# Kernel tuning notes

Measured on AMD Instinct MI355X. Metric: run time of the kernel, lower is better.

The kernel has to match this reference:

```python
import jax, jax.numpy as jnp
import numpy as np

H = 64  # hidden_layers

def _lstm_cell(x, h, c, Wih, Whh, bih, bhh):
    # PyTorch LSTMCell: gates ordered i, f, g, o
    gates = x @ Wih.T + bih + h @ Whh.T + bhh  # (B, 4H)
    i, f, g, o = jnp.split(gates, 4, axis=-1)
    c_new = jax.nn.sigmoid(f) * c + jax.nn.sigmoid(i) * jnp.tanh(g)
    h_new = jax.nn.sigmoid(o) * jnp.tanh(c_new)
    return h_new, c_new

def setup_inputs() -> dict:
    key = jax.random.key(0)
    ks = jax.random.split(key, 12)
    B, S = 1024, 512
    s1 = 1.0 / np.sqrt(H)
    u = lambda k, shape: jax.random.uniform(k, shape, jnp.float32, -s1, s1)
    return {
        "input_t": jax.random.normal(ks[0], (B, S), jnp.float32),
        "W_ih1": u(ks[1], (4 * H, 1)),
        "W_hh1": u(ks[2], (4 * H, H)),
        "b_ih1": u(ks[3], (4 * H,)),
        "b_hh1": u(ks[4], (4 * H,)),
        "W_ih2": u(ks[5], (4 * H, H)),
        "W_hh2": u(ks[6], (4 * H, H)),
        "b_ih2": u(ks[7], (4 * H,)),
        "b_hh2": u(ks[8], (4 * H,)),
        "W_lin": u(ks[9], (1, H)),
        "b_lin": u(ks[10], (1,)),
        "future_preds": 0,
    }

def reference(input_t, W_ih1, W_hh1, b_ih1, b_hh1, W_ih2, W_hh2, b_ih2, b_hh2,
              W_lin, b_lin, future_preds):
    B = input_t.shape[0]
    z = jnp.zeros((B, H), jnp.float32)

    def step(carry, x_t):
        h1, c1, h2, c2 = carry
        h1, c1 = _lstm_cell(x_t, h1, c1, W_ih1, W_hh1, b_ih1, b_hh1)
        h2, c2 = _lstm_cell(h1, h2, c2, W_ih2, W_hh2, b_ih2, b_hh2)
        out = h2 @ W_lin.T + b_lin  # (B, 1)
        return (h1, c1, h2, c2), out[:, 0]

    xs = input_t.T[:, :, None]  # (S, B, 1)
    carry, outs = jax.lax.scan(step, (z, z, z, z), xs)
    outputs = outs.T  # (B, S)

    if future_preds > 0:  # static Python int
        def step_ar(carry_o, _):
            (h1, c1, h2, c2), out = carry_o
            h1, c1 = _lstm_cell(out, h1, c1, W_ih1, W_hh1, b_ih1, b_hh1)
            h2, c2 = _lstm_cell(h1, h2, c2, W_ih2, W_hh2, b_ih2, b_hh2)
            out = h2 @ W_lin.T + b_lin
            return ((h1, c1, h2, c2), out), out[:, 0]

        last = outs[-1][:, None]  # (B, 1)
        _, outs2 = jax.lax.scan(step_ar, (carry, last), None, length=future_preds)
        outputs = jnp.concatenate([outputs, outs2.T], axis=1)
    return outputs
```

## Files before the change

### kernel.cpp

```cpp
#include <hip/hip_runtime.h>
#include <stdint.h>

#define HD   64
#define SEQ  512
#define BTCH 1024
#define NB   16
#define NBLK (BTCH / NB)
#define HSTR 72
#define XSTR 513

typedef _Float16 f16x8 __attribute__((ext_vector_type(8)));
typedef float    f32x4 __attribute__((ext_vector_type(4)));

union FragU { uint32_t u[4]; uint4 q; f16x8 v; };

static __device__ __forceinline__ float rcpf_(float x) {
#if __has_builtin(__builtin_amdgcn_rcpf)
    return __builtin_amdgcn_rcpf(x);
#else
    return 1.0f / x;
#endif
}
static __device__ __forceinline__ float sigmoidf_(float x) {
    return rcpf_(1.0f + __expf(-x));
}
static __device__ __forceinline__ float tanhf_(float x) {
    float e = __expf(2.0f * x);
    return (e - 1.0f) * rcpf_(e + 1.0f);
}
static __device__ __forceinline__ uint32_t pack2h(float a, float b) {
    _Float16 ha = (_Float16)a, hb = (_Float16)b;
    uint16_t ua = __builtin_bit_cast(uint16_t, ha);
    uint16_t ub = __builtin_bit_cast(uint16_t, hb);
    return (uint32_t)ua | ((uint32_t)ub << 16);
}

static __device__ __forceinline__ f16x8 make_frag(const float* __restrict__ W,
                                                  int row, int kb) {
    const float* p = W + row * HD + kb;
    FragU f;
    f.u[0] = pack2h(p[0], p[1]);
    f.u[1] = pack2h(p[2], p[3]);
    f.u[2] = pack2h(p[4], p[5]);
    f.u[3] = pack2h(p[6], p[7]);
    return f.v;
}

static __device__ __forceinline__ f16x8 read_B(const uint16_t* Hb, int n, int kb) {
    FragU f;
    f.q = *(const uint4*)(Hb + n * HSTR + kb);
    return f.v;
}

__global__ __attribute__((amdgpu_flat_work_group_size(512, 512)))
void lstm_mfma(const float* __restrict__ input,
               const float* __restrict__ Wih1,
               const float* __restrict__ Whh1,
               const float* __restrict__ bih1, const float* __restrict__ bhh1,
               const float* __restrict__ Wih2,
               const float* __restrict__ Whh2,
               const float* __restrict__ bih2, const float* __restrict__ bhh2,
               const float* __restrict__ Wlin,
               const float* __restrict__ blin,
               float* __restrict__ out)
{
    const int tid  = threadIdx.x;
    const int lane = tid & 63;
    const int wv   = tid >> 6;
    const int ub   = wv & 3;
    const int kc   = wv >> 2;
    const int n    = lane & 15;
    const int l4   = lane >> 4;
    const int b0   = blockIdx.x * NB;

    __shared__ float    xbuf[NB * XSTR];
    __shared__ float    obuf[NB * XSTR];
    __shared__ uint16_t H1[NB * HSTR];
    __shared__ uint16_t H2[NB * HSTR];
    __shared__ f32x4    xchg[4][4][64];
    __shared__ float    perW[4][16];

    for (int i = tid; i < NB * SEQ; i += 512) {
        int nn = i >> 9, tt = i & 511;
        xbuf[nn * XSTR + tt] = input[(size_t)(b0 + nn) * SEQ + tt];
    }
    for (int i = tid; i < NB * HSTR; i += 512) { H1[i] = 0; H2[i] = 0; }

    const int kb = kc * 32 + l4 * 8;
    f16x8 A1[4], A2[4], A3[4];
#pragma unroll
    for (int g = 0; g < 4; ++g) {
        int row = (g * 4 + ub) * 16 + n;
        A1[g] = make_frag(Whh1, row, kb);
        A2[g] = make_frag(Wih2, row, kb);
        A3[g] = make_frag(Whh2, row, kb);
    }

    const int u0 = ub * 16 + l4 * 4;
    f32x4 bias1f[4], wih1f[4], bias2f[4];
    if (kc == 1) {
#pragma unroll
        for (int g = 0; g < 4; ++g)
#pragma unroll
            for (int r = 0; r < 4; ++r) {
                int row = g * 64 + u0 + r;
                bias1f[g][r] = bih1[row] + bhh1[row];
                wih1f[g][r]  = Wih1[row];
            }
    } else {
#pragma unroll
        for (int g = 0; g < 4; ++g)
#pragma unroll
            for (int r = 0; r < 4; ++r) {
                int row = g * 64 + u0 + r;
                bias2f[g][r] = bih2[row] + bhh2[row];
            }
    }
    float wl0 = 0.f, wl1 = 0.f, wl2 = 0.f, wl3 = 0.f;
    if (kc == 0) { wl0 = Wlin[u0]; wl1 = Wlin[u0 + 1]; wl2 = Wlin[u0 + 2]; wl3 = Wlin[u0 + 3]; }
    const float bl = blin[0];
    float c1[4] = {0.f, 0.f, 0.f, 0.f};
    float c2[4] = {0.f, 0.f, 0.f, 0.f};
    const f32x4 zero4 = {0.f, 0.f, 0.f, 0.f};

    __syncthreads();

#pragma unroll 1
    for (int t = 0; t < SEQ; ++t) {
        f16x8 B1 = read_B(H1, n, kb);
        f32x4 acc[4];
        if (kc == 1) {
            float x = xbuf[n * XSTR + t];
#pragma unroll
            for (int g = 0; g < 4; ++g) acc[g] = bias1f[g] + x * wih1f[g];
        } else {
#pragma unroll
            for (int g = 0; g < 4; ++g) acc[g] = zero4;
        }
#pragma unroll
        for (int g = 0; g < 4; ++g)
            acc[g] = __builtin_amdgcn_mfma_f32_16x16x32_f16(A1[g], B1, acc[g], 0, 0, 0);

        if (kc == 1) {
#pragma unroll
            for (int g = 0; g < 4; ++g) xchg[ub][g][lane] = acc[g];
        }
        __syncthreads();

        if (kc == 0) {
#pragma unroll
            for (int g = 0; g < 4; ++g) acc[g] += xchg[ub][g][lane];
            float h1v[4];
#pragma unroll
            for (int r = 0; r < 4; ++r) {
                float i_ = sigmoidf_(acc[0][r]);
                float f_ = sigmoidf_(acc[1][r]);
                float g_ = tanhf_(acc[2][r]);
                float o_ = sigmoidf_(acc[3][r]);
                c1[r] = f_ * c1[r] + i_ * g_;
                h1v[r] = o_ * tanhf_(c1[r]);
            }
            uint2 hw; hw.x = pack2h(h1v[0], h1v[1]); hw.y = pack2h(h1v[2], h1v[3]);
            *(uint2*)(&H1[n * HSTR + u0]) = hw;
        }
        __syncthreads();

        f16x8 B2 = read_B(H1, n, kb);
        f16x8 B3 = read_B(H2, n, kb);
        if (kc == 0) {
#pragma unroll
            for (int g = 0; g < 4; ++g) acc[g] = bias2f[g];
        } else {
#pragma unroll
            for (int g = 0; g < 4; ++g) acc[g] = zero4;
        }
#pragma unroll
        for (int g = 0; g < 4; ++g) {
            acc[g] = __builtin_amdgcn_mfma_f32_16x16x32_f16(A2[g], B2, acc[g], 0, 0, 0);
            acc[g] = __builtin_amdgcn_mfma_f32_16x16x32_f16(A3[g], B3, acc[g], 0, 0, 0);
        }
        if (kc == 1) {
#pragma unroll
            for (int g = 0; g < 4; ++g) xchg[ub][g][lane] = acc[g];
        }
        __syncthreads();

        if (kc == 0) {
#pragma unroll
            for (int g = 0; g < 4; ++g) acc[g] += xchg[ub][g][lane];
            float h2v[4];
#pragma unroll
            for (int r = 0; r < 4; ++r) {
                float i_ = sigmoidf_(acc[0][r]);
                float f_ = sigmoidf_(acc[1][r]);
                float g_ = tanhf_(acc[2][r]);
                float o_ = sigmoidf_(acc[3][r]);
                c2[r] = f_ * c2[r] + i_ * g_;
                h2v[r] = o_ * tanhf_(c2[r]);
            }
            uint2 hw; hw.x = pack2h(h2v[0], h2v[1]); hw.y = pack2h(h2v[2], h2v[3]);
            *(uint2*)(&H2[n * HSTR + u0]) = hw;
            float p = h2v[0] * wl0 + h2v[1] * wl1 + h2v[2] * wl2 + h2v[3] * wl3;
            p += __shfl_xor(p, 16, 64);
            p += __shfl_xor(p, 32, 64);
            if (l4 == 0) perW[ub][n] = p;
        }
        __syncthreads();

        if (wv == 0) {
            float s = perW[0][n] + perW[1][n] + perW[2][n] + perW[3][n] + bl;
            if (lane < 16) obuf[n * XSTR + t] = s;
        }
    }

    __syncthreads();
    for (int i = tid; i < NB * SEQ; i += 512) {
        int nn = i >> 9, tt = i & 511;
        out[(size_t)(b0 + nn) * SEQ + tt] = obuf[nn * XSTR + tt];
    }
}

extern "C" void kernel_launch(void* const* d_in, const int* in_sizes, int n_in,
                              void* d_out, int out_size, void* d_ws, size_t ws_size,
                              hipStream_t stream) {
    const float* input = (const float*)d_in[0];
    const float* Wih1  = (const float*)d_in[1];
    const float* Whh1  = (const float*)d_in[2];
    const float* bih1  = (const float*)d_in[3];
    const float* bhh1  = (const float*)d_in[4];
    const float* Wih2  = (const float*)d_in[5];
    const float* Whh2  = (const float*)d_in[6];
    const float* bih2  = (const float*)d_in[7];
    const float* bhh2  = (const float*)d_in[8];
    const float* Wlin  = (const float*)d_in[9];
    const float* blin  = (const float*)d_in[10];

    float* outp = (float*)d_out;

    lstm_mfma<<<dim3(NBLK), dim3(512), 0, stream>>>(
        input, Wih1, Whh1, bih1, bhh1, Wih2, Whh2, bih2, bhh2, Wlin, blin, outp);
}
```

Measured before the change: 834.5 us.

## Replace K-split reduction with redundant full-K MMA per wave pair

Each pair of waves now computes the full 64-wide K reduction on its own, doubling the MFMA work, instead of splitting K across the pair and exchanging partial sums through shared memory. The gate nonlinearity work is split so each wave handles two of the four output rows. This removes the xchg round-trip and one barrier per step, and lets all waves do useful activation work. Input is now read directly from global memory, prefetched one step ahead, and outputs are written straight to global, which drops the large shared staging buffers. The kernel is also pinned to two waves per EU; the costs are twice the register footprint for the A fragments and many small uncoalesced global stores.

```diff
diff --git a/kernel.cpp b/kernel.cpp
--- a/kernel.cpp
+++ b/kernel.cpp
@@ -7,7 +7,6 @@
 #define NB   16
 #define NBLK (BTCH / NB)
 #define HSTR 72
-#define XSTR 513
 
 typedef _Float16 f16x8 __attribute__((ext_vector_type(8)));
 typedef float    f32x4 __attribute__((ext_vector_type(4)));
@@ -52,7 +51,8 @@
     return f.v;
 }
 
-__global__ __attribute__((amdgpu_flat_work_group_size(512, 512)))
+__global__ __attribute__((amdgpu_flat_work_group_size(512, 512),
+                          amdgpu_waves_per_eu(2, 2)))
 void lstm_mfma(const float* __restrict__ input,
                const float* __restrict__ Wih1,
                const float* __restrict__ Whh1,
@@ -68,155 +68,117 @@
     const int lane = tid & 63;
     const int wv   = tid >> 6;
     const int ub   = wv & 3;
-    const int kc   = wv >> 2;
+    const int hf   = wv >> 2;
     const int n    = lane & 15;
     const int l4   = lane >> 4;
     const int b0   = blockIdx.x * NB;
-
-    __shared__ float    xbuf[NB * XSTR];
-    __shared__ float    obuf[NB * XSTR];
+    const int u0   = ub * 16 + l4 * 4;
+
     __shared__ uint16_t H1[NB * HSTR];
     __shared__ uint16_t H2[NB * HSTR];
-    __shared__ f32x4    xchg[4][4][64];
-    __shared__ float    perW[4][16];
-
-    for (int i = tid; i < NB * SEQ; i += 512) {
-        int nn = i >> 9, tt = i & 511;
-        xbuf[nn * XSTR + tt] = input[(size_t)(b0 + nn) * SEQ + tt];
-    }
+    __shared__ float    perW[8][16];
+
     for (int i = tid; i < NB * HSTR; i += 512) { H1[i] = 0; H2[i] = 0; }
 
-    const int kb = kc * 32 + l4 * 8;
-    f16x8 A1[4], A2[4], A3[4];
+    f16x8 A1[4][2], A2[4][2], A3[4][2];
 #pragma unroll
     for (int g = 0; g < 4; ++g) {
         int row = (g * 4 + ub) * 16 + n;
-        A1[g] = make_frag(Whh1, row, kb);
-        A2[g] = make_frag(Wih2, row, kb);
-        A3[g] = make_frag(Whh2, row, kb);
+#pragma unroll
+        for (int h = 0; h < 2; ++h) {
+            int kb = h * 32 + l4 * 8;
+            A1[g][h] = make_frag(Whh1, row, kb);
+            A2[g][h] = make_frag(Wih2, row, kb);
+            A3[g][h] = make_frag(Whh2, row, kb);
+        }
     }
 
-    const int u0 = ub * 16 + l4 * 4;
     f32x4 bias1f[4], wih1f[4], bias2f[4];
-    if (kc == 1) {
-#pragma unroll
-        for (int g = 0; g < 4; ++g)
-#pragma unroll
-            for (int r = 0; r < 4; ++r) {
-                int row = g * 64 + u0 + r;
-                bias1f[g][r] = bih1[row] + bhh1[row];
-                wih1f[g][r]  = Wih1[row];
-            }
-    } else {
-#pragma unroll
-        for (int g = 0; g < 4; ++g)
-#pragma unroll
-            for (int r = 0; r < 4; ++r) {
-                int row = g * 64 + u0 + r;
-                bias2f[g][r] = bih2[row] + bhh2[row];
-            }
-    }
-    float wl0 = 0.f, wl1 = 0.f, wl2 = 0.f, wl3 = 0.f;
-    if (kc == 0) { wl0 = Wlin[u0]; wl1 = Wlin[u0 + 1]; wl2 = Wlin[u0 + 2]; wl3 = Wlin[u0 + 3]; }
-    const float bl = blin[0];
-    float c1[4] = {0.f, 0.f, 0.f, 0.f};
-    float c2[4] = {0.f, 0.f, 0.f, 0.f};
-    const f32x4 zero4 = {0.f, 0.f, 0.f, 0.f};
-
+#pragma unroll
+    for (int g = 0; g < 4; ++g)
+#pragma unroll
+        for (int r = 0; r < 4; ++r) {
+            int row = g * 64 + u0 + r;
+            bias1f[g][r] = bih1[row] + bhh1[row];
+            wih1f[g][r]  = Wih1[row];
+            bias2f[g][r] = bih2[row] + bhh2[row];
+        }
+    const float wl0 = Wlin[u0 + hf * 2];
+    const float wl1 = Wlin[u0 + hf * 2 + 1];
+    const float bl  = blin[0];
+
+    float c1[2] = {0.f, 0.f};
+    float c2[2] = {0.f, 0.f};
+
+    const float* xp = input + (size_t)(b0 + n) * SEQ;
+    float xn = xp[0];
+
+    const int klo = l4 * 8, khi = 32 + l4 * 8;
     __syncthreads();
 
 #pragma unroll 1
     for (int t = 0; t < SEQ; ++t) {
-        f16x8 B1 = read_B(H1, n, kb);
+        const float x = xn;
+        xn = xp[(t + 1) & (SEQ - 1)];
+
+        f16x8 B1l = read_B(H1, n, klo), B1h = read_B(H1, n, khi);
+        f16x8 B3l = read_B(H2, n, klo), B3h = read_B(H2, n, khi);
         f32x4 acc[4];
-        if (kc == 1) {
-            float x = xbuf[n * XSTR + t];
-#pragma unroll
-            for (int g = 0; g < 4; ++g) acc[g] = bias1f[g] + x * wih1f[g];
-        } else {
-#pragma unroll
-            for (int g = 0; g < 4; ++g) acc[g] = zero4;
-        }
-#pragma unroll
-        for (int g = 0; g < 4; ++g)
-            acc[g] = __builtin_amdgcn_mfma_f32_16x16x32_f16(A1[g], B1, acc[g], 0, 0, 0);
-
-        if (kc == 1) {
-#pragma unroll
-            for (int g = 0; g < 4; ++g) xchg[ub][g][lane] = acc[g];
+#pragma unroll
+        for (int g = 0; g < 4; ++g) {
+            acc[g] = bias1f[g] + x * wih1f[g];
+            acc[g] = __builtin_amdgcn_mfma_f32_16x16x32_f16(A1[g][0], B1l, acc[g], 0, 0, 0);
+            acc[g] = __builtin_amdgcn_mfma_f32_16x16x32_f16(A1[g][1], B1h, acc[g], 0, 0, 0);
+        }
+        float h1v[2];
+#pragma unroll
+        for (int rr = 0; rr < 2; ++rr) {
+            int r = hf * 2 + rr;
+            float i_ = sigmoidf_(acc[0][r]);
+            float f_ = sigmoidf_(acc[1][r]);
+            float g_ = tanhf_(acc[2][r]);
+            float o_ = sigmoidf_(acc[3][r]);
+            c1[rr] = f_ * c1[rr] + i_ * g_;
+            h1v[rr] = o_ * tanhf_(c1[rr]);
         }
         __syncthreads();
 
-        if (kc == 0) {
-#pragma unroll
-            for (int g = 0; g < 4; ++g) acc[g] += xchg[ub][g][lane];
-            float h1v[4];
-#pragma unroll
-            for (int r = 0; r < 4; ++r) {
-                float i_ = sigmoidf_(acc[0][r]);
-                float f_ = sigmoidf_(acc[1][r]);
-                float g_ = tanhf_(acc[2][r]);
-                float o_ = sigmoidf_(acc[3][r]);
-                c1[r] = f_ * c1[r] + i_ * g_;
-                h1v[r] = o_ * tanhf_(c1[r]);
-            }
-            uint2 hw; hw.x = pack2h(h1v[0], h1v[1]); hw.y = pack2h(h1v[2], h1v[3]);
-            *(uint2*)(&H1[n * HSTR + u0]) = hw;
-        }
+        *(uint32_t*)(&H1[n * HSTR + u0 + hf * 2]) = pack2h(h1v[0], h1v[1]);
         __syncthreads();
 
-        f16x8 B2 = read_B(H1, n, kb);
-        f16x8 B3 = read_B(H2, n, kb);
-        if (kc == 0) {
-#pragma unroll
-            for (int g = 0; g < 4; ++g) acc[g] = bias2f[g];
-        } else {
-#pragma unroll
-            for (int g = 0; g < 4; ++g) acc[g] = zero4;
-        }
+        f16x8 B2l = read_B(H1, n, klo), B2h = read_B(H1, n, khi);
 #pragma unroll
         for (int g = 0; g < 4; ++g) {
-            acc[g] = __builtin_amdgcn_mfma_f32_16x16x32_f16(A2[g], B2, acc[g], 0, 0, 0);
-            acc[g] = __builtin_amdgcn_mfma_f32_16x16x32_f16(A3[g], B3, acc[g], 0, 0, 0);
-        }
-        if (kc == 1) {
-#pragma unroll
-            for (int g = 0; g < 4; ++g) xchg[ub][g][lane] = acc[g];
-        }
+            acc[g] = bias2f[g];
+            acc[g] = __builtin_amdgcn_mfma_f32_16x16x32_f16(A2[g][0], B2l, acc[g], 0, 0, 0);
+            acc[g] = __builtin_amdgcn_mfma_f32_16x16x32_f16(A2[g][1], B2h, acc[g], 0, 0, 0);
+            acc[g] = __builtin_amdgcn_mfma_f32_16x16x32_f16(A3[g][0], B3l, acc[g], 0, 0, 0);
+            acc[g] = __builtin_amdgcn_mfma_f32_16x16x32_f16(A3[g][1], B3h, acc[g], 0, 0, 0);
+        }
+        float h2v[2];
+#pragma unroll
+        for (int rr = 0; rr < 2; ++rr) {
+            int r = hf * 2 + rr;
+            float i_ = sigmoidf_(acc[0][r]);
+            float f_ = sigmoidf_(acc[1][r]);
+            float g_ = tanhf_(acc[2][r]);
+            float o_ = sigmoidf_(acc[3][r]);
+            c2[rr] = f_ * c2[rr] + i_ * g_;
+            h2v[rr] = o_ * tanhf_(c2[rr]);
+        }
+        *(uint32_t*)(&H2[n * HSTR + u0 + hf * 2]) = pack2h(h2v[0], h2v[1]);
+
+        float p = h2v[0] * wl0 + h2v[1] * wl1;
+        p += __shfl_xor(p, 16, 64);
+        p += __shfl_xor(p, 32, 64);
+        if (l4 == 0) perW[wv][n] = p;
         __syncthreads();
 
-        if (kc == 0) {
-#pragma unroll
-            for (int g = 0; g < 4; ++g) acc[g] += xchg[ub][g][lane];
-            float h2v[4];
-#pragma unroll
-            for (int r = 0; r < 4; ++r) {
-                float i_ = sigmoidf_(acc[0][r]);
-                float f_ = sigmoidf_(acc[1][r]);
-                float g_ = tanhf_(acc[2][r]);
-                float o_ = sigmoidf_(acc[3][r]);
-                c2[r] = f_ * c2[r] + i_ * g_;
-                h2v[r] = o_ * tanhf_(c2[r]);
-            }
-            uint2 hw; hw.x = pack2h(h2v[0], h2v[1]); hw.y = pack2h(h2v[2], h2v[3]);
-            *(uint2*)(&H2[n * HSTR + u0]) = hw;
-            float p = h2v[0] * wl0 + h2v[1] * wl1 + h2v[2] * wl2 + h2v[3] * wl3;
-            p += __shfl_xor(p, 16, 64);
-            p += __shfl_xor(p, 32, 64);
-            if (l4 == 0) perW[ub][n] = p;
-        }
-        __syncthreads();
-
-        if (wv == 0) {
-            float s = perW[0][n] + perW[1][n] + perW[2][n] + perW[3][n] + bl;
-            if (lane < 16) obuf[n * XSTR + t] = s;
-        }
-    }
-
-    __syncthreads();
-    for (int i = tid; i < NB * SEQ; i += 512) {
-        int nn = i >> 9, tt = i & 511;
-        out[(size_t)(b0 + nn) * SEQ + tt] = obuf[nn * XSTR + tt];
+        if (wv == 0 && lane < 16) {
+            float s = perW[0][n] + perW[1][n] + perW[2][n] + perW[3][n]
+                    + perW[4][n] + perW[5][n] + perW[6][n] + perW[7][n] + bl;
+            out[(size_t)(b0 + n) * SEQ + t] = s;
+        }
     }
 }
 
```

Measured after the change: 809.5 us. -3.0%, faster.
